# Kernel tuning notes

Hardware: AMD Instinct MI355X
Metric: run time of the kernel (lower is better)

## Reference

```python
import jax, jax.numpy as jnp
import numpy as np

HIDDEN = 1024
NUM_BLOCKS = 8
BLOCK = HIDDEN // NUM_BLOCKS  # 128
EPS = 1e-6


def cayley_batch(A):
    # A: [b, r, r] -> orthogonal Q = (I - S) @ inv(I + S + eps*I), S = 0.5*(A - A^T)
    b, r, _ = A.shape
    I = jnp.eye(r, dtype=A.dtype)
    S = 0.5 * (A - jnp.swapaxes(A, -2, -1))
    return jnp.matmul(I - S, jnp.linalg.inv(I + S + EPS * I))


def apply_block_diag(W, R):
    # W @ block_diag(R_0..R_{n-1}) without materializing the hidden x hidden matrix.
    # W: [out, hidden], R: [n, bs, bs]
    out = W.shape[0]
    Wb = W.reshape(out, NUM_BLOCKS, BLOCK)
    return jnp.einsum('onb,nbc->onc', Wb, R).reshape(out, NUM_BLOCKS * BLOCK)


def setup_inputs() -> dict:
    key = jax.random.key(0)
    ks = jax.random.split(key, 6)
    return {
        'attn_weight': jax.random.normal(ks[0], (3 * HIDDEN, HIDDEN), dtype=jnp.float32) * 0.02,
        'bias': jax.random.normal(ks[1], (3 * HIDDEN,), dtype=jnp.float32) * 0.02,
        'x': jax.random.normal(ks[2], (8, 4096, HIDDEN), dtype=jnp.float32),
        'q_R': jax.random.normal(ks[3], (NUM_BLOCKS, BLOCK, BLOCK), dtype=jnp.float32),
        'k_R': jax.random.normal(ks[4], (NUM_BLOCKS, BLOCK, BLOCK), dtype=jnp.float32),
        'v_R': jax.random.normal(ks[5], (NUM_BLOCKS, BLOCK, BLOCK), dtype=jnp.float32),
    }


def reference(attn_weight, bias, x, q_R, k_R, v_R):
    orth_q = cayley_batch(q_R)
    orth_k = cayley_batch(k_R)
    orth_v = cayley_batch(v_R)
    q_w, k_w, v_w = jnp.split(attn_weight, 3, axis=0)  # each [hidden, hidden]
    filt_q = apply_block_diag(q_w, orth_q)
    filt_k = apply_block_diag(k_w, orth_k)
    filt_v = apply_block_diag(v_w, orth_v)
    filt = jnp.concatenate([filt_q, filt_k, filt_v], axis=0)  # [3*hidden, hidden]
    # F.linear: x @ filt^T + bias -> [B, S, 3*hidden]
    return jnp.einsum('bsh,oh->bso', x, filt) + bias
```

## Files before the change

### kernel.cpp

```cpp
#include <hip/hip_runtime.h>

typedef __bf16 bf16x8 __attribute__((ext_vector_type(8)));
typedef float  f32x4  __attribute__((ext_vector_type(4)));

#define EPSC 1e-6f

__device__ __forceinline__ unsigned short f2bf(float f) {
  union { float f; unsigned int u; } c; c.f = f;
  unsigned int u = c.u;
  u = u + 0x7FFFu + ((u >> 16) & 1u);
  return (unsigned short)(u >> 16);
}
__device__ __forceinline__ float bf2f(unsigned short h) {
  union { unsigned int u; float f; } c; c.u = ((unsigned int)h) << 16;
  return c.f;
}
__device__ __forceinline__ void gl_lds16(const unsigned short* g, unsigned short* l) {
  __builtin_amdgcn_global_load_lds((const __attribute__((address_space(1))) void*)g,
                                   (__attribute__((address_space(3))) void*)l, 16, 0, 0);
}

template<int N> __device__ __forceinline__ void waitvm() {
  if constexpr (N == 8)      asm volatile("s_waitcnt vmcnt(8)" ::: "memory");
  else if constexpr (N == 4) asm volatile("s_waitcnt vmcnt(4)" ::: "memory");
  else                       asm volatile("s_waitcnt vmcnt(0)" ::: "memory");
}

__global__ void __launch_bounds__(512) cayley_cvt_k(const float* __restrict__ qR,
                                                    const float* __restrict__ kR,
                                                    const float* __restrict__ vR,
                                                    float* __restrict__ wsL,
                                                    float* __restrict__ wsQt,
                                                    const float4* __restrict__ xin,
                                                    ushort4* __restrict__ xbf,
                                                    int n4) {
  extern __shared__ float A_s[];
  const int tid = threadIdx.x;

  if (blockIdx.x >= 24) {
    int i = (blockIdx.x - 24) * 512 + tid;
    int stride = (gridDim.x - 24) * 512;
    for (; i < n4; i += stride) {
      float4 v = xin[i];
      ushort4 o;
      o.x = f2bf(v.x); o.y = f2bf(v.y); o.z = f2bf(v.z); o.w = f2bf(v.w);
      xbf[i] = o;
    }
    return;
  }

  float4* A4 = (float4*)A_s;
  const int m = blockIdx.x;
  const float* R = (m < 8 ? qR : (m < 16 ? kR : vR)) + (size_t)(m & 7) * 16384;
  float* Lg = wsL  + (size_t)m * 16384;
  float* Qt = wsQt + (size_t)m * 16384;

  for (int idx = tid; idx < 16384; idx += 512) {
    int i = idx >> 7, j = idx & 127;
    float s = 0.5f * (R[idx] - R[j * 128 + i]);
    float v = ((i == j) ? (1.0f + EPSC) : 0.0f) - s;
    A_s[idx] = v;
    Lg[idx] = v;
  }

  const int c = tid & 31;
  const int rg = tid >> 5;
  for (int k = 0; k < 128; ++k) {
    __syncthreads();
    if (tid < 32) {
      float ip = 1.0f / A_s[k * 128 + k];
      float4 v = A4[k * 32 + tid];
      v.x *= ip; v.y *= ip; v.z *= ip; v.w *= ip;
      if (tid == (k >> 2)) {
        int k3 = k & 3;
        if (k3 == 0) v.x = ip; else if (k3 == 1) v.y = ip;
        else if (k3 == 2) v.z = ip; else v.w = ip;
      }
      A4[k * 32 + tid] = v;
    }
    __syncthreads();

    float4 rk = A4[k * 32 + c];
    const int kc = k >> 2, k3 = k & 3;
    const float ipv = (k3 == 0) ? rk.x : (k3 == 1) ? rk.y : (k3 == 2) ? rk.z : rk.w;

    float mi[8];
    float4 v[8];
#pragma unroll
    for (int p = 0; p < 8; ++p) mi[p] = A_s[(p * 16 + rg) * 128 + k];
#pragma unroll
    for (int p = 0; p < 8; ++p) v[p] = A4[(p * 16 + rg) * 32 + c];
#pragma unroll
    for (int p = 0; p < 8; ++p) {
      const int i = p * 16 + rg;
      const bool isk = (i == k);
      const float mm = isk ? 0.0f : mi[p];
      float4 w = v[p];
      w.x -= mm * rk.x; w.y -= mm * rk.y; w.z -= mm * rk.z; w.w -= mm * rk.w;
      if (c == kc && !isk) {
        const float fx = -mm * ipv;
        if (k3 == 0) w.x = fx; else if (k3 == 1) w.y = fx;
        else if (k3 == 2) w.z = fx; else w.w = fx;
      }
      A4[i * 32 + c] = w;
    }
  }
  __syncthreads();

  const int ti = tid >> 4, tj = tid & 15;
  const int i0 = ti * 4, j0 = tj * 8;
  float acc[4][8];
#pragma unroll
  for (int r = 0; r < 4; ++r)
#pragma unroll
    for (int s = 0; s < 8; ++s) acc[r][s] = 0.f;

  for (int tc = 0; tc < 32; ++tc) {
    float4 b4[8];
#pragma unroll
    for (int s = 0; s < 8; ++s)
      b4[s] = *(const float4*)&Lg[(size_t)(j0 + s) * 128 + tc * 4];
#pragma unroll
    for (int r = 0; r < 4; ++r) {
      float4 a4 = A4[(i0 + r) * 32 + tc];
#pragma unroll
      for (int s = 0; s < 8; ++s)
        acc[r][s] += a4.x * b4[s].x + a4.y * b4[s].y + a4.z * b4[s].z + a4.w * b4[s].w;
    }
  }
#pragma unroll
  for (int r = 0; r < 4; ++r)
#pragma unroll
    for (int s = 0; s < 8; ++s) {
      float v = acc[r][s] - EPSC * A_s[(i0 + r) * 128 + j0 + s];
      Qt[(size_t)(i0 + r) * 128 + j0 + s] = v;
    }
}

__global__ void __launch_bounds__(256) filt_k(const float* __restrict__ W,
                                              const float* __restrict__ wsQt,
                                              unsigned short* __restrict__ filt) {
  __shared__ unsigned short Qs[128 * 136];
  const int m = blockIdx.x;
  const int ot = blockIdx.y;
  const int mset = m >> 3, n = m & 7;
  const float* Qt = wsQt + (size_t)m * 16384;
  const int tid = threadIdx.x;

  for (int idx = tid; idx < 16384; idx += 256) {
    int i = idx >> 7, j = idx & 127;
    Qs[i * 136 + j] = f2bf(Qt[idx]);
  }
  __syncthreads();

  const int ol = tid & 63, cg = tid >> 6;
  const int go = mset * 1024 + ot * 64 + ol;
  const float* Wrow = W + (size_t)go * 1024 + n * 128;

  float acc[32];
#pragma unroll
  for (int i = 0; i < 32; ++i) acc[i] = 0.f;

  for (int b4 = 0; b4 < 32; ++b4) {
    float4 w4 = *(const float4*)(Wrow + b4 * 4);
#pragma unroll
    for (int cc = 0; cc < 32; ++cc) {
      int cidx = cg * 32 + cc;
      ushort4 q4 = *(const ushort4*)&Qs[cidx * 136 + b4 * 4];
      acc[cc] += w4.x * bf2f(q4.x) + w4.y * bf2f(q4.y)
               + w4.z * bf2f(q4.z) + w4.w * bf2f(q4.w);
    }
  }
  unsigned short* dst = filt + (size_t)go * 1024 + n * 128 + cg * 32;
#pragma unroll
  for (int g2 = 0; g2 < 8; ++g2) {
    ushort4 o;
    o.x = f2bf(acc[g2 * 4 + 0]); o.y = f2bf(acc[g2 * 4 + 1]);
    o.z = f2bf(acc[g2 * 4 + 2]); o.w = f2bf(acc[g2 * 4 + 3]);
    *(ushort4*)(dst + g2 * 4) = o;
  }
}

__global__ void __launch_bounds__(512, 2) gemm_k(const unsigned short* __restrict__ Ax,
                                                 const unsigned short* __restrict__ Bf,
                                                 const float* __restrict__ bias,
                                                 float* __restrict__ C) {
  extern __shared__ char smem_g[];
  const int tid = threadIdx.x;
  const int lane = tid & 63, wave = tid >> 6;
  const int wm = wave & 1, wn = wave >> 1;
  const int quad = lane >> 4, l16 = lane & 15;
  const long mbase = (long)blockIdx.y * 256;
  const long nbase = (long)blockIdx.x * 256;

  const unsigned short* gA0; const unsigned short* gA1;
  const unsigned short* gB0; const unsigned short* gB1;
  int dof0, dof1;
  {
    int D0 = 0 * 8192 + tid * 16;
    int D1 = 1 * 8192 + tid * 16;
    int L0 = D0 ^ (((D0 >> 7) & 3) << 4);
    int L1 = D1 ^ (((D1 >> 7) & 3) << 4);
    int r0 = L0 >> 6, c0 = (L0 & 63) >> 1;
    int r1 = L1 >> 6, c1 = (L1 & 63) >> 1;
    gA0 = Ax + (size_t)(mbase + r0) * 1024 + c0;
    gA1 = Ax + (size_t)(mbase + r1) * 1024 + c1;
    gB0 = Bf + (size_t)(nbase + r0) * 1024 + c0;
    gB1 = Bf + (size_t)(nbase + r1) * 1024 + c1;
    dof0 = D0; dof1 = D1;
  }

  int aoff[8], boff[4];
#pragma unroll
  for (int mi = 0; mi < 8; ++mi) {
    int row = wm * 128 + mi * 16 + l16;
    int L = row * 64 + quad * 16;
    aoff[mi] = L ^ (((L >> 7) & 3) << 4);
  }
#pragma unroll
  for (int ni = 0; ni < 4; ++ni) {
    int row = wn * 64 + ni * 16 + l16;
    int L = row * 64 + quad * 16;
    boff[ni] = 16384 + (L ^ (((L >> 7) & 3) << 4));
  }

  f32x4 acc[8][4];
#pragma unroll
  for (int mi = 0; mi < 8; ++mi)
#pragma unroll
    for (int ni = 0; ni < 4; ++ni) {
      acc[mi][ni][0] = 0.f; acc[mi][ni][1] = 0.f;
      acc[mi][ni][2] = 0.f; acc[mi][ni][3] = 0.f;
    }

#define GSTAGE(T)                                                              \
  {                                                                            \
    char* sb = smem_g + ((T) & 3) * 32768;                                     \
    gl_lds16(gA0 + (T) * 32, (unsigned short*)(sb + dof0));                    \
    gl_lds16(gA1 + (T) * 32, (unsigned short*)(sb + dof1));                    \
    gl_lds16(gB0 + (T) * 32, (unsigned short*)(sb + 16384 + dof0));            \
    gl_lds16(gB1 + (T) * 32, (unsigned short*)(sb + 16384 + dof1));            \
  }

#define GSTEP(T, VM)                                                           \
  {                                                                            \
    waitvm<VM>();                                                              \
    __builtin_amdgcn_s_barrier();                                              \
    asm volatile("" ::: "memory");                                             \
    const char* bb = smem_g + ((T) & 3) * 32768;                               \
    bf16x8 bfr[4], afr[8];                                                     \
    _Pragma("unroll")                                                          \
    for (int ni = 0; ni < 4; ++ni) bfr[ni] = *(const bf16x8*)(bb + boff[ni]);  \
    _Pragma("unroll")                                                          \
    for (int mi = 0; mi < 8; ++mi) afr[mi] = *(const bf16x8*)(bb + aoff[mi]);  \
    __builtin_amdgcn_s_setprio(1);                                             \
    _Pragma("unroll")                                                          \
    for (int mi = 0; mi < 8; ++mi)                                             \
      _Pragma("unroll")                                                        \
      for (int ni = 0; ni < 4; ++ni)                                           \
        acc[mi][ni] = __builtin_amdgcn_mfma_f32_16x16x32_bf16(                 \
            afr[mi], bfr[ni], acc[mi][ni], 0, 0, 0);                           \
    __builtin_amdgcn_s_setprio(0);                                             \
  }

  GSTAGE(0);
  GSTAGE(1);

  for (int t = 0; t < 30; ++t) {
    GSTAGE(t + 2);
    GSTEP(t, 8);
  }
  GSTEP(30, 4);
  GSTEP(31, 0);

#undef GSTAGE
#undef GSTEP

#pragma unroll
  for (int ni = 0; ni < 4; ++ni) {
    long gcol = nbase + wn * 64 + ni * 16 + l16;
    float bv = bias[gcol];
#pragma unroll
    for (int mi = 0; mi < 8; ++mi) {
      long grow = mbase + wm * 128 + mi * 16 + quad * 4;
#pragma unroll
      for (int r = 0; r < 4; ++r)
        C[(grow + r) * 3072 + gcol] = acc[mi][ni][r] + bv;
    }
  }
}

extern "C" void kernel_launch(void* const* d_in, const int* in_sizes, int n_in,
                              void* d_out, int out_size, void* d_ws, size_t ws_size,
                              hipStream_t stream) {
  const float* W    = (const float*)d_in[0];
  const float* bias = (const float*)d_in[1];
  const float* x    = (const float*)d_in[2];
  const float* qR   = (const float*)d_in[3];
  const float* kR   = (const float*)d_in[4];
  const float* vR   = (const float*)d_in[5];
  float* out = (float*)d_out;

  char* ws = (char*)d_ws;
  float* wsL           = (float*)(ws);
  float* wsQt          = (float*)(ws + 1572864);
  unsigned short* wsF  = (unsigned short*)(ws + 3145728);
  unsigned short* wsX  = (unsigned short*)(ws + 9437184);

  static bool attr_done = false;
  if (!attr_done) {
    (void)hipFuncSetAttribute(reinterpret_cast<const void*>(gemm_k),
                              hipFuncAttributeMaxDynamicSharedMemorySize, 131072);
    attr_done = true;
  }

  cayley_cvt_k<<<24 + 2048, 512, 65536, stream>>>(qR, kR, vR, wsL, wsQt,
                                                  (const float4*)x, (ushort4*)wsX,
                                                  33554432 / 4);
  filt_k<<<dim3(24, 16), 256, 0, stream>>>(W, wsQt, wsF);
  gemm_k<<<dim3(12, 128), 512, 131072, stream>>>(wsX, wsF, bias, out);
}
```

Baseline: 872.1 us.

## Split GEMM K-step into two phases with deeper prefetch and interleaved staging

Restructures the bf16 MFMA main loop so each K-tile runs in two half-phases. Each half loads part of the B fragments, issues half of the next global->LDS stage, then runs 16 MFMAs between barriers. Prefetch depth rises from 2 to 3 tiles in flight across the 4-buffer ring. The goal is to spread LDS reads and global loads between MFMA bursts and hide more memory latency, in the style of ping-pong scheduling. The cost is extra barriers per tile, and tighter ring reuse raises the risk of buffer hazards.

```diff
diff --git a/kernel.cpp b/kernel.cpp
--- a/kernel.cpp
+++ b/kernel.cpp
@@ -18,12 +18,6 @@
 __device__ __forceinline__ void gl_lds16(const unsigned short* g, unsigned short* l) {
   __builtin_amdgcn_global_load_lds((const __attribute__((address_space(1))) void*)g,
                                    (__attribute__((address_space(3))) void*)l, 16, 0, 0);
-}
-
-template<int N> __device__ __forceinline__ void waitvm() {
-  if constexpr (N == 8)      asm volatile("s_waitcnt vmcnt(8)" ::: "memory");
-  else if constexpr (N == 4) asm volatile("s_waitcnt vmcnt(4)" ::: "memory");
-  else                       asm volatile("s_waitcnt vmcnt(0)" ::: "memory");
 }
 
 __global__ void __launch_bounds__(512) cayley_cvt_k(const float* __restrict__ qR,
@@ -233,48 +227,82 @@
       acc[mi][ni][2] = 0.f; acc[mi][ni][3] = 0.f;
     }
 
-#define GSTAGE(T)                                                              \
+  bf16x8 afr[8], bfr[4];
+
+#define STAGE_A(T)                                                             \
   {                                                                            \
     char* sb = smem_g + ((T) & 3) * 32768;                                     \
     gl_lds16(gA0 + (T) * 32, (unsigned short*)(sb + dof0));                    \
     gl_lds16(gA1 + (T) * 32, (unsigned short*)(sb + dof1));                    \
+  }
+#define STAGE_B(T)                                                             \
+  {                                                                            \
+    char* sb = smem_g + ((T) & 3) * 32768;                                     \
     gl_lds16(gB0 + (T) * 32, (unsigned short*)(sb + 16384 + dof0));            \
     gl_lds16(gB1 + (T) * 32, (unsigned short*)(sb + 16384 + dof1));            \
   }
 
-#define GSTEP(T, VM)                                                           \
-  {                                                                            \
-    waitvm<VM>();                                                              \
+#define MFMA_HALF(NL)                                                          \
+  {                                                                            \
+    asm volatile("s_waitcnt lgkmcnt(0)" ::: "memory");                         \
+    __builtin_amdgcn_sched_barrier(0);                                         \
+    __builtin_amdgcn_s_setprio(1);                                             \
+    _Pragma("unroll")                                                          \
+    for (int mi = 0; mi < 8; ++mi) {                                           \
+      acc[mi][NL] = __builtin_amdgcn_mfma_f32_16x16x32_bf16(                   \
+          afr[mi], bfr[NL], acc[mi][NL], 0, 0, 0);                             \
+      acc[mi][(NL) + 1] = __builtin_amdgcn_mfma_f32_16x16x32_bf16(             \
+          afr[mi], bfr[(NL) + 1], acc[mi][(NL) + 1], 0, 0, 0);                 \
+    }                                                                          \
+    __builtin_amdgcn_s_setprio(0);                                             \
     __builtin_amdgcn_s_barrier();                                              \
-    asm volatile("" ::: "memory");                                             \
+  }
+
+#define PHASE_A(T, DOSTAGE)                                                    \
+  {                                                                            \
     const char* bb = smem_g + ((T) & 3) * 32768;                               \
-    bf16x8 bfr[4], afr[8];                                                     \
-    _Pragma("unroll")                                                          \
-    for (int ni = 0; ni < 4; ++ni) bfr[ni] = *(const bf16x8*)(bb + boff[ni]);  \
     _Pragma("unroll")                                                          \
     for (int mi = 0; mi < 8; ++mi) afr[mi] = *(const bf16x8*)(bb + aoff[mi]);  \
-    __builtin_amdgcn_s_setprio(1);                                             \
-    _Pragma("unroll")                                                          \
-    for (int mi = 0; mi < 8; ++mi)                                             \
-      _Pragma("unroll")                                                        \
-      for (int ni = 0; ni < 4; ++ni)                                           \
-        acc[mi][ni] = __builtin_amdgcn_mfma_f32_16x16x32_bf16(                 \
-            afr[mi], bfr[ni], acc[mi][ni], 0, 0, 0);                           \
-    __builtin_amdgcn_s_setprio(0);                                             \
-  }
-
-  GSTAGE(0);
-  GSTAGE(1);
-
-  for (int t = 0; t < 30; ++t) {
-    GSTAGE(t + 2);
-    GSTEP(t, 8);
-  }
-  GSTEP(30, 4);
-  GSTEP(31, 0);
-
-#undef GSTAGE
-#undef GSTEP
+    bfr[0] = *(const bf16x8*)(bb + boff[0]);                                   \
+    bfr[1] = *(const bf16x8*)(bb + boff[1]);                                   \
+    if (DOSTAGE) STAGE_A((T) + 3);                                             \
+    __builtin_amdgcn_s_barrier();                                              \
+    MFMA_HALF(0)                                                               \
+  }
+
+#define PHASE_B(T, DOSTAGE, VMSTR)                                             \
+  {                                                                            \
+    const char* bb = smem_g + ((T) & 3) * 32768;                               \
+    bfr[2] = *(const bf16x8*)(bb + boff[2]);                                   \
+    bfr[3] = *(const bf16x8*)(bb + boff[3]);                                   \
+    if (DOSTAGE) STAGE_B((T) + 3);                                             \
+    asm volatile(VMSTR ::: "memory");                                          \
+    __builtin_amdgcn_s_barrier();                                              \
+    MFMA_HALF(2)                                                               \
+  }
+
+  STAGE_A(0); STAGE_B(0);
+  STAGE_A(1); STAGE_B(1);
+  STAGE_A(2); STAGE_B(2);
+  asm volatile("s_waitcnt vmcnt(8)" ::: "memory");
+  __builtin_amdgcn_s_barrier();
+
+  for (int t = 0; t < 29; ++t) {
+    PHASE_A(t, 1)
+    PHASE_B(t, 1, "s_waitcnt vmcnt(8)")
+  }
+  PHASE_A(29, 0)
+  PHASE_B(29, 0, "s_waitcnt vmcnt(4)")
+  PHASE_A(30, 0)
+  PHASE_B(30, 0, "s_waitcnt vmcnt(0)")
+  PHASE_A(31, 0)
+  PHASE_B(31, 0, "s_nop 0")
+
+#undef PHASE_A
+#undef PHASE_B
+#undef MFMA_HALF
+#undef STAGE_A
+#undef STAGE_B
 
 #pragma unroll
   for (int ni = 0; ni < 4; ++ni) {
```

Result: no change. 858.4 us (-1.6%).
